# Performance work log

Hardware: AMD Instinct MI355X
Metric: run time of the kernel (lower is better)

The kernel has to match this reference:

```python
import jax, jax.numpy as jnp
import numpy as np

B, T, C = 256, 256, 147
BPM, H_DIM, NH = 32, 64, 4
HD = H_DIM // NH


def setup_inputs() -> dict:
    key = jax.random.key(0)
    ks = jax.random.split(key, 12)
    def lin(k, fan_in, fan_out):
        bound = 1.0 / np.sqrt(fan_in)
        kw, kb = jax.random.split(k)
        W = jax.random.uniform(kw, (fan_in, fan_out), jnp.float32, -bound, bound)
        b = jax.random.uniform(kb, (fan_out,), jnp.float32, -bound, bound)
        return W, b
    Wq, bq = lin(ks[0], C, H_DIM)
    Wk, bk = lin(ks[1], C, H_DIM)
    Wv, bv = lin(ks[2], C, H_DIM)
    Wb, bb = lin(ks[3], BPM, H_DIM)
    Wo, bo = lin(ks[4], H_DIM, C)
    pose = jax.random.normal(ks[5], (B, T, C), jnp.float32)
    bpm_emb = jax.random.normal(ks[6], (B, BPM), jnp.float32)
    return {"pose": pose, "bpm_emb": bpm_emb,
            "Wq": Wq, "bq": bq, "Wk": Wk, "bk": bk, "Wv": Wv, "bv": bv,
            "Wb": Wb, "bb": bb, "Wo": Wo, "bo": bo}


def reference(pose, bpm_emb, Wq, bq, Wk, bk, Wv, bv, Wb, bb, Wo, bo):
    Bb, Tt, Cc = pose.shape
    scale = HD ** -0.5
    # projections -> [B, H, T, hd]
    def split_heads(x):
        return x.reshape(Bb, Tt, NH, HD).transpose(0, 2, 1, 3)
    q = split_heads(pose @ Wq + bq)
    k = split_heads(pose @ Wk + bk)
    v = split_heads(pose @ Wv + bv)
    # bpm-conditioned key bias: [B, H, 1, hd]
    bpm_feat = (bpm_emb @ Wb + bb).reshape(Bb, 1, NH, HD).transpose(0, 2, 1, 3)
    k = k + bpm_feat
    # attention
    scores = jnp.einsum('bhqd,bhkd->bhqk', q, k) * scale
    attn = jax.nn.softmax(scores, axis=-1)
    out = jnp.einsum('bhqk,bhkd->bhqd', attn, v)
    out = out.transpose(0, 2, 1, 3).reshape(Bb, Tt, NH * HD)
    return out @ Wo + bo
```

## Files before the change

### kernel.cpp

```cpp
#include <hip/hip_runtime.h>

constexpr int kC = 147, kH = 64, kHD = 16, kBPM = 32;

typedef __attribute__((ext_vector_type(8)))  short bf16x8;
typedef __attribute__((ext_vector_type(4)))  float f32x4;
typedef __attribute__((ext_vector_type(16))) float f32x16;
typedef __attribute__((ext_vector_type(4)))  short s16x4;

__device__ __forceinline__ short f2bf(float f) {
    unsigned u = __builtin_bit_cast(unsigned, f);
    u += 0x7fffu + ((u >> 16) & 1u);
    return (short)(u >> 16);
}
#define MFMA16(a,b,c) __builtin_amdgcn_mfma_f32_16x16x32_bf16((a),(b),(c),0,0,0)
#define MFMA32(a,b,c) __builtin_amdgcn_mfma_f32_32x32x16_bf16((a),(b),(c),0,0,0)

#if __has_builtin(__builtin_amdgcn_exp2f)
  #define EXP2(x) __builtin_amdgcn_exp2f(x)
#else
  #define EXP2(x) __expf((x) * 0.6931471805599453f)
#endif
constexpr float kQScale = 0.25f * 1.4426950408889634f;

constexpr int QS  = 72;
constexpr int VS  = 264;
constexpr int PS  = 40;
constexpr int WSS = 168;
constexpr int WOS = 72;

__device__ __forceinline__ void stage_w_qkv(const float* __restrict__ W,
                                            float scale, short* Ws, int tid) {
    #pragma unroll
    for (int it = 0; it < 5; ++it) {
        const int i = it * 1024 + tid;
        const int c = i & 63, k = (i >> 6) * 2;
        const float v0 = (k     < kC) ? W[k * kH + c] * scale : 0.f;
        const float v1 = (k + 1 < kC) ? W[(k + 1) * kH + c] * scale : 0.f;
        const unsigned pack = (unsigned)(unsigned short)f2bf(v0)
                            | ((unsigned)(unsigned short)f2bf(v1) << 16);
        *(unsigned*)&Ws[c * WSS + (k ^ (((c >> 3) & 3) << 3))] = pack;
    }
}

__global__ __launch_bounds__(1024, 4) void fused_kernel(
    const float* __restrict__ pose, const float* __restrict__ bpm_emb,
    const float* __restrict__ Wq, const float* __restrict__ bq,
    const float* __restrict__ Wk, const float* __restrict__ bk,
    const float* __restrict__ Wv, const float* __restrict__ bv,
    const float* __restrict__ Wb, const float* __restrict__ bb,
    const float* __restrict__ Wo, const float* __restrict__ bo,
    float* __restrict__ out)
{
    __shared__ __align__(16) short qs[256 * QS];
    __shared__ __align__(16) short ks_[256 * QS];
    __shared__ __align__(16) short vt[kH * VS];
    __shared__ __align__(16) short WsPt[20480];
    __shared__ float l_s[16 * 64];
    __shared__ float bias_s[192];
    short* const Ws = WsPt;
    short* const Pt = WsPt;

    const int tid = threadIdx.x;
    const int w = tid >> 6, lane = tid & 63;
    const int ll = lane & 15, lq = lane >> 4;
    const int lm = lane & 31, lh = lane >> 5;
    const int b = blockIdx.x;
    const size_t pbase = (size_t)b * 256 * kC;

    bf16x8 pf[5];
    {
        const int row = w * 16 + ll;
        const float* prow = pose + pbase + (size_t)row * kC;
        #pragma unroll
        for (int ksp = 0; ksp < 5; ++ksp) {
            const int c0 = ksp * 32 + lq * 8;
            float v[8];
            if (c0 + 8 <= kC) {
                const float4 f0 = *(const float4*)(prow + c0);
                const float4 f1 = *(const float4*)(prow + c0 + 4);
                v[0]=f0.x; v[1]=f0.y; v[2]=f0.z; v[3]=f0.w;
                v[4]=f1.x; v[5]=f1.y; v[6]=f1.z; v[7]=f1.w;
            } else {
                #pragma unroll
                for (int e = 0; e < 8; ++e) v[e] = (c0 + e < kC) ? prow[c0 + e] : 0.f;
            }
            bf16x8 t;
            #pragma unroll
            for (int e = 0; e < 8; ++e) t[e] = f2bf(v[e]);
            pf[ksp] = t;
        }
    }
    if (tid < 192) {
        const int m = tid >> 6, c = tid & 63;
        float a = ((m == 0) ? bq : (m == 1) ? bk : bv)[c];
        if (m == 1) {
            a += bb[c];
            #pragma unroll
            for (int k2 = 0; k2 < kBPM; ++k2)
                a = fmaf(bpm_emb[b * kBPM + k2], Wb[k2 * kH + c], a);
        }
        if (m == 0) a *= kQScale;
        bias_s[tid] = a;
    }
    stage_w_qkv(Wq, kQScale, Ws, tid);
    __syncthreads();

    for (int m = 0; m < 3; ++m) {
        f32x4 acc[4];
        #pragma unroll
        for (int mt = 0; mt < 4; ++mt) acc[mt] = (f32x4){0.f,0.f,0.f,0.f};
        #pragma unroll
        for (int ksp = 0; ksp < 5; ++ksp)
            #pragma unroll
            for (int mt = 0; mt < 4; ++mt) {
                const int c = mt * 16 + ll;
                const int key = ((c >> 3) & 3) << 3;
                const bf16x8 wf = *(const bf16x8*)(Ws + c * WSS + ((ksp*32 + lq*8) ^ key));
                acc[mt] = MFMA16(wf, pf[ksp], acc[mt]);
            }
        __syncthreads();
        if (m == 0)      stage_w_qkv(Wk, 1.0f, Ws, tid);
        else if (m == 1) stage_w_qkv(Wv, 1.0f, Ws, tid);
        const int row = w * 16 + ll;
        #pragma unroll
        for (int mt = 0; mt < 4; ++mt) {
            const int c0 = mt * 16 + 4 * lq;
            const float4 bv4 = *(const float4*)&bias_s[m * kH + c0];
            if (m < 2) {
                s16x4 pk;
                pk[0] = f2bf(acc[mt][0] + bv4.x);
                pk[1] = f2bf(acc[mt][1] + bv4.y);
                pk[2] = f2bf(acc[mt][2] + bv4.z);
                pk[3] = f2bf(acc[mt][3] + bv4.w);
                *(s16x4*)((m == 0 ? qs : ks_) + row * QS + c0) = pk;
            } else {
                vt[(c0 + 0) * VS + row] = f2bf(acc[mt][0] + bv4.x);
                vt[(c0 + 1) * VS + row] = f2bf(acc[mt][1] + bv4.y);
                vt[(c0 + 2) * VS + row] = f2bf(acc[mt][2] + bv4.z);
                vt[(c0 + 3) * VS + row] = f2bf(acc[mt][3] + bv4.w);
            }
        }
        __syncthreads();
    }

    const int h = w & 3;
    const int q0 = (w >> 2) * 64;
    bf16x8 qf[2];
    #pragma unroll
    for (int s32 = 0; s32 < 2; ++s32)
        qf[s32] = *(const bf16x8*)(qs + (q0 + s32*32 + lm) * QS + h*16 + lh*8);

    f32x4 oacc[2][2];
    #pragma unroll
    for (int s32 = 0; s32 < 2; ++s32) {
        oacc[s32][0] = (f32x4){0.f,0.f,0.f,0.f};
        oacc[s32][1] = (f32x4){0.f,0.f,0.f,0.f};
    }
    float lp[2] = {0.f, 0.f};
    short* Pw = Pt + w * 32 * PS;
    const int wkey = ((lm >> 3) & 3) << 3;

    for (int jb = 0; jb < 8; ++jb) {
        const int j0 = jb * 32;
        const bf16x8 kf = *(const bf16x8*)(ks_ + (j0 + lm) * QS + h*16 + lh*8);
        const bf16x8 vf = *(const bf16x8*)(vt + (h*16 + ll) * VS + j0 + lq*8);
        #pragma unroll
        for (int s32 = 0; s32 < 2; ++s32) {
            const f32x16 z16 = {0.f,0.f,0.f,0.f,0.f,0.f,0.f,0.f,
                                0.f,0.f,0.f,0.f,0.f,0.f,0.f,0.f};
            const f32x16 s = MFMA32(kf, qf[s32], z16);
            float sum = 0.f;
            #pragma unroll
            for (int g = 0; g < 4; ++g) {
                const float p0 = EXP2(s[4*g + 0]);
                const float p1 = EXP2(s[4*g + 1]);
                const float p2 = EXP2(s[4*g + 2]);
                const float p3 = EXP2(s[4*g + 3]);
                sum += (p0 + p1) + (p2 + p3);
                s16x4 pk; pk[0] = f2bf(p0); pk[1] = f2bf(p1);
                pk[2] = f2bf(p2); pk[3] = f2bf(p3);
                *(s16x4*)(Pw + lm * PS + ((8*g + 4*lh) ^ wkey)) = pk;
            }
            lp[s32] += sum;
            #pragma unroll
            for (int half = 0; half < 2; ++half) {
                const int qp = half * 16 + ll;
                const int rkey = ((qp >> 3) & 3) << 3;
                const bf16x8 pfr = *(const bf16x8*)(Pw + qp * PS + ((lq*8) ^ rkey));
                oacc[s32][half] = MFMA16(vf, pfr, oacc[s32][half]);
            }
        }
    }
    #pragma unroll
    for (int s32 = 0; s32 < 2; ++s32) {
        const float l2 = lp[s32] + __shfl_xor(lp[s32], 32);
        if (lane < 32) l_s[w * 64 + s32 * 32 + lm] = l2;
    }
    #pragma unroll
    for (int s32 = 0; s32 < 2; ++s32)
        #pragma unroll
        for (int half = 0; half < 2; ++half) {
            const int qi = s32 * 32 + half * 16 + ll;
            const float inv = 1.f / l_s[w * 64 + qi];
            s16x4 pk;
            #pragma unroll
            for (int r = 0; r < 4; ++r) pk[r] = f2bf(oacc[s32][half][r] * inv);
            *(s16x4*)(qs + (q0 + qi) * QS + h*16 + 4*lq) = pk;
        }
    __syncthreads();

    #pragma unroll
    for (int it = 0; it < 5; ++it) {
        const int i = it * 1024 + tid;
        const int n = i % 160, k = (i / 160) * 2;
        const float v0 = (n < kC) ? Wo[k * kC + n] : 0.f;
        const float v1 = (n < kC) ? Wo[(k + 1) * kC + n] : 0.f;
        const unsigned pack = (unsigned)(unsigned short)f2bf(v0)
                            | ((unsigned)(unsigned short)f2bf(v1) << 16);
        *(unsigned*)&Ws[n * WOS + (k ^ (((n >> 3) & 3) << 3))] = pack;
    }
    __syncthreads();

    bf16x8 xf[2];
    #pragma unroll
    for (int k2 = 0; k2 < 2; ++k2)
        xf[k2] = *(const bf16x8*)(qs + (w*16 + ll) * QS + k2*32 + lq*8);

    f32x4 po[10];
    #pragma unroll
    for (int mt = 0; mt < 10; ++mt) po[mt] = (f32x4){0.f,0.f,0.f,0.f};
    #pragma unroll
    for (int k2 = 0; k2 < 2; ++k2)
        #pragma unroll
        for (int mt = 0; mt < 10; ++mt) {
            const int n = mt * 16 + ll;
            const int key = ((n >> 3) & 3) << 3;
            const bf16x8 wf = *(const bf16x8*)(Ws + n * WOS + ((k2*32 + lq*8) ^ key));
            po[mt] = MFMA16(wf, xf[k2], po[mt]);
        }
    {
        const int row = w * 16 + ll;
        float* orow = out + ((size_t)b * 256 + row) * kC;
        #pragma unroll
        for (int mt = 0; mt < 10; ++mt) {
            const int c0 = mt * 16 + 4 * lq;
            if (mt < 9) {
                const float4 bv4 = *(const float4*)(bo + c0);
                float4 o;
                o.x = po[mt][0] + bv4.x; o.y = po[mt][1] + bv4.y;
                o.z = po[mt][2] + bv4.z; o.w = po[mt][3] + bv4.w;
                *(float4*)(orow + c0) = o;
            } else {
                #pragma unroll
                for (int r = 0; r < 4; ++r) {
                    const int c = c0 + r;
                    if (c < kC) orow[c] = po[mt][r] + bo[c];
                }
            }
        }
    }
}

extern "C" void kernel_launch(void* const* d_in, const int* in_sizes, int n_in,
                              void* d_out, int out_size, void* d_ws, size_t ws_size,
                              hipStream_t stream) {
    const float* pose    = (const float*)d_in[0];
    const float* bpm_emb = (const float*)d_in[1];
    const float* Wq = (const float*)d_in[2];  const float* bq = (const float*)d_in[3];
    const float* Wk = (const float*)d_in[4];  const float* bk = (const float*)d_in[5];
    const float* Wv = (const float*)d_in[6];  const float* bv = (const float*)d_in[7];
    const float* Wb = (const float*)d_in[8];  const float* bb = (const float*)d_in[9];
    const float* Wo = (const float*)d_in[10]; const float* bo = (const float*)d_in[11];
    float* out = (float*)d_out;

    fused_kernel<<<256, 1024, 0, stream>>>(
        pose, bpm_emb, Wq, bq, Wk, bk, Wv, bv, Wb, bb, Wo, bo, out);
}
```

Baseline: 134.7 us.

## Split fused attention kernel into QKV projection and attention kernels via workspace

Splits the single fused per-batch kernel (256 blocks of 1024 threads) into two kernels, each with 512 blocks of 512 threads. The first computes Q, K and transposed V for half a sequence per block and writes them as bf16 to global workspace. The second computes attention plus the output projection for half the queries, reading K and V directly from global memory. This is meant to double the block count for better CU fill and cut per-block LDS use, at the cost of a global round trip for Q/K/V, a second launch, and Wo being staged twice per batch.

```diff
diff --git a/kernel.cpp b/kernel.cpp
--- a/kernel.cpp
+++ b/kernel.cpp
@@ -1,6 +1,6 @@
 #include <hip/hip_runtime.h>
 
-constexpr int kC = 147, kH = 64, kHD = 16, kBPM = 32;
+constexpr int kC = 147, kH = 64, kBPM = 32;
 
 typedef __attribute__((ext_vector_type(8)))  short bf16x8;
 typedef __attribute__((ext_vector_type(4)))  float f32x4;
@@ -23,7 +23,7 @@
 constexpr float kQScale = 0.25f * 1.4426950408889634f;
 
 constexpr int QS  = 72;
-constexpr int VS  = 264;
+constexpr int VSA = 136;
 constexpr int PS  = 40;
 constexpr int WSS = 168;
 constexpr int WOS = 72;
@@ -31,8 +31,8 @@
 __device__ __forceinline__ void stage_w_qkv(const float* __restrict__ W,
                                             float scale, short* Ws, int tid) {
     #pragma unroll
-    for (int it = 0; it < 5; ++it) {
-        const int i = it * 1024 + tid;
+    for (int it = 0; it < 10; ++it) {
+        const int i = it * 512 + tid;
         const int c = i & 63, k = (i >> 6) * 2;
         const float v0 = (k     < kC) ? W[k * kH + c] * scale : 0.f;
         const float v1 = (k + 1 < kC) ? W[(k + 1) * kH + c] * scale : 0.f;
@@ -42,34 +42,27 @@
     }
 }
 
-__global__ __launch_bounds__(1024, 4) void fused_kernel(
+__global__ __launch_bounds__(512, 4) void qkv_kernel(
     const float* __restrict__ pose, const float* __restrict__ bpm_emb,
     const float* __restrict__ Wq, const float* __restrict__ bq,
     const float* __restrict__ Wk, const float* __restrict__ bk,
     const float* __restrict__ Wv, const float* __restrict__ bv,
     const float* __restrict__ Wb, const float* __restrict__ bb,
-    const float* __restrict__ Wo, const float* __restrict__ bo,
-    float* __restrict__ out)
+    short* __restrict__ q_g, short* __restrict__ k_g, short* __restrict__ vT_g)
 {
-    __shared__ __align__(16) short qs[256 * QS];
-    __shared__ __align__(16) short ks_[256 * QS];
-    __shared__ __align__(16) short vt[kH * VS];
-    __shared__ __align__(16) short WsPt[20480];
-    __shared__ float l_s[16 * 64];
+    __shared__ __align__(16) short Ws[64 * WSS];
+    __shared__ __align__(16) short vt[64 * VSA];
     __shared__ float bias_s[192];
-    short* const Ws = WsPt;
-    short* const Pt = WsPt;
 
     const int tid = threadIdx.x;
     const int w = tid >> 6, lane = tid & 63;
     const int ll = lane & 15, lq = lane >> 4;
-    const int lm = lane & 31, lh = lane >> 5;
-    const int b = blockIdx.x;
+    const int b = blockIdx.x >> 1, half = blockIdx.x & 1;
     const size_t pbase = (size_t)b * 256 * kC;
+    const int row = half * 128 + w * 16 + ll;
 
     bf16x8 pf[5];
     {
-        const int row = w * 16 + ll;
         const float* prow = pose + pbase + (size_t)row * kC;
         #pragma unroll
         for (int ksp = 0; ksp < 5; ++ksp) {
@@ -121,7 +114,6 @@
         __syncthreads();
         if (m == 0)      stage_w_qkv(Wk, 1.0f, Ws, tid);
         else if (m == 1) stage_w_qkv(Wv, 1.0f, Ws, tid);
-        const int row = w * 16 + ll;
         #pragma unroll
         for (int mt = 0; mt < 4; ++mt) {
             const int c0 = mt * 16 + 4 * lq;
@@ -132,23 +124,54 @@
                 pk[1] = f2bf(acc[mt][1] + bv4.y);
                 pk[2] = f2bf(acc[mt][2] + bv4.z);
                 pk[3] = f2bf(acc[mt][3] + bv4.w);
-                *(s16x4*)((m == 0 ? qs : ks_) + row * QS + c0) = pk;
+                short* dst = (m == 0) ? q_g : k_g;
+                *(s16x4*)(dst + ((size_t)b * 256 + row) * kH + c0) = pk;
             } else {
-                vt[(c0 + 0) * VS + row] = f2bf(acc[mt][0] + bv4.x);
-                vt[(c0 + 1) * VS + row] = f2bf(acc[mt][1] + bv4.y);
-                vt[(c0 + 2) * VS + row] = f2bf(acc[mt][2] + bv4.z);
-                vt[(c0 + 3) * VS + row] = f2bf(acc[mt][3] + bv4.w);
+                const int jloc = w * 16 + ll;
+                vt[(c0 + 0) * VSA + jloc] = f2bf(acc[mt][0] + bv4.x);
+                vt[(c0 + 1) * VSA + jloc] = f2bf(acc[mt][1] + bv4.y);
+                vt[(c0 + 2) * VSA + jloc] = f2bf(acc[mt][2] + bv4.z);
+                vt[(c0 + 3) * VSA + jloc] = f2bf(acc[mt][3] + bv4.w);
             }
         }
         __syncthreads();
     }
 
-    const int h = w & 3;
-    const int q0 = (w >> 2) * 64;
+    {
+        const int d = tid >> 3, j16 = (tid & 7) * 16;
+        const short* src = vt + d * VSA + j16;
+        short* dst = vT_g + ((size_t)b * kH + d) * 256 + half * 128 + j16;
+        *(int4*)(dst)     = *(const int4*)(src);
+        *(int4*)(dst + 8) = *(const int4*)(src + 8);
+    }
+}
+
+__global__ __launch_bounds__(512, 4) void attn_kernel(
+    const short* __restrict__ q_g, const short* __restrict__ k_g,
+    const short* __restrict__ vT_g,
+    const float* __restrict__ Wo, const float* __restrict__ bo,
+    float* __restrict__ out)
+{
+    __shared__ __align__(16) short X[128 * QS];
+    __shared__ __align__(16) short WsPt[160 * WOS];
+    __shared__ float l_s[8 * 64];
+    short* const Ws = WsPt;
+    short* const Pt = WsPt;
+
+    const int tid = threadIdx.x;
+    const int w = tid >> 6, lane = tid & 63;
+    const int ll = lane & 15, lq = lane >> 4;
+    const int lm = lane & 31, lh = lane >> 5;
+    const int b = blockIdx.x >> 1, qh = blockIdx.x & 1;
+    const int h = w & 3, qsel = w >> 2;
+    const int qrow0 = qh * 128 + qsel * 64;
+    const size_t kvbase = (size_t)b * 256 * kH;
+
     bf16x8 qf[2];
     #pragma unroll
     for (int s32 = 0; s32 < 2; ++s32)
-        qf[s32] = *(const bf16x8*)(qs + (q0 + s32*32 + lm) * QS + h*16 + lh*8);
+        qf[s32] = *(const bf16x8*)(q_g + kvbase
+                    + (size_t)(qrow0 + s32*32 + lm) * kH + h*16 + lh*8);
 
     f32x4 oacc[2][2];
     #pragma unroll
@@ -160,10 +183,13 @@
     short* Pw = Pt + w * 32 * PS;
     const int wkey = ((lm >> 3) & 3) << 3;
 
+    #pragma unroll 2
     for (int jb = 0; jb < 8; ++jb) {
         const int j0 = jb * 32;
-        const bf16x8 kf = *(const bf16x8*)(ks_ + (j0 + lm) * QS + h*16 + lh*8);
-        const bf16x8 vf = *(const bf16x8*)(vt + (h*16 + ll) * VS + j0 + lq*8);
+        const bf16x8 kf = *(const bf16x8*)(k_g + kvbase
+                            + (size_t)(j0 + lm) * kH + h*16 + lh*8);
+        const bf16x8 vf = *(const bf16x8*)(vT_g
+                            + ((size_t)b * kH + h*16 + ll) * 256 + j0 + lq*8);
         #pragma unroll
         for (int s32 = 0; s32 < 2; ++s32) {
             const f32x16 z16 = {0.f,0.f,0.f,0.f,0.f,0.f,0.f,0.f,
@@ -183,11 +209,11 @@
             }
             lp[s32] += sum;
             #pragma unroll
-            for (int half = 0; half < 2; ++half) {
-                const int qp = half * 16 + ll;
+            for (int hf = 0; hf < 2; ++hf) {
+                const int qp = hf * 16 + ll;
                 const int rkey = ((qp >> 3) & 3) << 3;
                 const bf16x8 pfr = *(const bf16x8*)(Pw + qp * PS + ((lq*8) ^ rkey));
-                oacc[s32][half] = MFMA16(vf, pfr, oacc[s32][half]);
+                oacc[s32][hf] = MFMA16(vf, pfr, oacc[s32][hf]);
             }
         }
     }
@@ -199,19 +225,19 @@
     #pragma unroll
     for (int s32 = 0; s32 < 2; ++s32)
         #pragma unroll
-        for (int half = 0; half < 2; ++half) {
-            const int qi = s32 * 32 + half * 16 + ll;
+        for (int hf = 0; hf < 2; ++hf) {
+            const int qi = s32 * 32 + hf * 16 + ll;
             const float inv = 1.f / l_s[w * 64 + qi];
             s16x4 pk;
             #pragma unroll
-            for (int r = 0; r < 4; ++r) pk[r] = f2bf(oacc[s32][half][r] * inv);
-            *(s16x4*)(qs + (q0 + qi) * QS + h*16 + 4*lq) = pk;
+            for (int r = 0; r < 4; ++r) pk[r] = f2bf(oacc[s32][hf][r] * inv);
+            *(s16x4*)(X + (qsel * 64 + qi) * QS + h*16 + 4*lq) = pk;
         }
     __syncthreads();
 
     #pragma unroll
-    for (int it = 0; it < 5; ++it) {
-        const int i = it * 1024 + tid;
+    for (int it = 0; it < 10; ++it) {
+        const int i = it * 512 + tid;
         const int n = i % 160, k = (i / 160) * 2;
         const float v0 = (n < kC) ? Wo[k * kC + n] : 0.f;
         const float v1 = (n < kC) ? Wo[(k + 1) * kC + n] : 0.f;
@@ -224,7 +250,7 @@
     bf16x8 xf[2];
     #pragma unroll
     for (int k2 = 0; k2 < 2; ++k2)
-        xf[k2] = *(const bf16x8*)(qs + (w*16 + ll) * QS + k2*32 + lq*8);
+        xf[k2] = *(const bf16x8*)(X + (w*16 + ll) * QS + k2*32 + lq*8);
 
     f32x4 po[10];
     #pragma unroll
@@ -239,8 +265,8 @@
             po[mt] = MFMA16(wf, xf[k2], po[mt]);
         }
     {
-        const int row = w * 16 + ll;
-        float* orow = out + ((size_t)b * 256 + row) * kC;
+        const int orow_i = qh * 128 + w * 16 + ll;
+        float* orow = out + ((size_t)b * 256 + orow_i) * kC;
         #pragma unroll
         for (int mt = 0; mt < 10; ++mt) {
             const int c0 = mt * 16 + 4 * lq;
@@ -273,6 +299,11 @@
     const float* Wo = (const float*)d_in[10]; const float* bo = (const float*)d_in[11];
     float* out = (float*)d_out;
 
-    fused_kernel<<<256, 1024, 0, stream>>>(
-        pose, bpm_emb, Wq, bq, Wk, bk, Wv, bv, Wb, bb, Wo, bo, out);
-}
+    short* q_g  = (short*)d_ws;
+    short* k_g  = q_g + (size_t)256 * 256 * kH;
+    short* vT_g = k_g + (size_t)256 * 256 * kH;
+
+    qkv_kernel<<<512, 512, 0, stream>>>(
+        pose, bpm_emb, Wq, bq, Wk, bk, Wv, bv, Wb, bb, q_g, k_g, vT_g);
+    attn_kernel<<<512, 512, 0, stream>>>(q_g, k_g, vT_g, Wo, bo, out);
+}
```

New measurement: 147.4 us. 9.4% more time.

## Prefetch weights into registers early and use hardware packed bf16 conversion

Applied to the files above, without the earlier changes.

Issues the global loads for Wq/Wk/Wv at kernel start and for Wo before the attention loop, holding them in registers so later LDS staging only converts and stores. This hides global-memory latency that previously stalled between phases. It also swaps the software round-to-nearest f2bf for the v_cvt_pk_bf16_f32 instruction in most places and unrolls the QKV and attention loops. The cost is about 40 extra live VGPRs per thread, which risks spilling under launch_bounds(1024,4).

```diff
diff --git a/kernel.cpp b/kernel.cpp
--- a/kernel.cpp
+++ b/kernel.cpp
@@ -1,16 +1,22 @@
 #include <hip/hip_runtime.h>
 
-constexpr int kC = 147, kH = 64, kHD = 16, kBPM = 32;
+constexpr int kC = 147, kH = 64, kBPM = 32;
 
 typedef __attribute__((ext_vector_type(8)))  short bf16x8;
 typedef __attribute__((ext_vector_type(4)))  float f32x4;
 typedef __attribute__((ext_vector_type(16))) float f32x16;
-typedef __attribute__((ext_vector_type(4)))  short s16x4;
+typedef __attribute__((ext_vector_type(2)))  unsigned u32x2;
+typedef __attribute__((ext_vector_type(4)))  unsigned u32x4;
 
 __device__ __forceinline__ short f2bf(float f) {
     unsigned u = __builtin_bit_cast(unsigned, f);
     u += 0x7fffu + ((u >> 16) & 1u);
     return (short)(u >> 16);
+}
+__device__ __forceinline__ unsigned cvt_pk(float lo, float hi) {
+    unsigned r;
+    asm("v_cvt_pk_bf16_f32 %0, %1, %2" : "=v"(r) : "v"(lo), "v"(hi));
+    return r;
 }
 #define MFMA16(a,b,c) __builtin_amdgcn_mfma_f32_16x16x32_bf16((a),(b),(c),0,0,0)
 #define MFMA32(a,b,c) __builtin_amdgcn_mfma_f32_32x32x16_bf16((a),(b),(c),0,0,0)
@@ -28,17 +34,14 @@
 constexpr int WSS = 168;
 constexpr int WOS = 72;
 
-__device__ __forceinline__ void stage_w_qkv(const float* __restrict__ W,
-                                            float scale, short* Ws, int tid) {
+__device__ __forceinline__ void stage_w_regs(const float* wr ,
+                                             short* Ws, int tid) {
     #pragma unroll
     for (int it = 0; it < 5; ++it) {
         const int i = it * 1024 + tid;
         const int c = i & 63, k = (i >> 6) * 2;
-        const float v0 = (k     < kC) ? W[k * kH + c] * scale : 0.f;
-        const float v1 = (k + 1 < kC) ? W[(k + 1) * kH + c] * scale : 0.f;
-        const unsigned pack = (unsigned)(unsigned short)f2bf(v0)
-                            | ((unsigned)(unsigned short)f2bf(v1) << 16);
-        *(unsigned*)&Ws[c * WSS + (k ^ (((c >> 3) & 3) << 3))] = pack;
+        *(unsigned*)&Ws[c * WSS + (k ^ (((c >> 3) & 3) << 3))]
+            = cvt_pk(wr[2*it], wr[2*it + 1]);
     }
 }
 
@@ -67,6 +70,20 @@
     const int b = blockIdx.x;
     const size_t pbase = (size_t)b * 256 * kC;
 
+    float wq_r[10], wk_r[10], wv_r[10];
+    #pragma unroll
+    for (int it = 0; it < 5; ++it) {
+        const int i = it * 1024 + tid;
+        const int c = i & 63, k = (i >> 6) * 2;
+        const bool b0 = k < kC, b1 = k + 1 < kC;
+        wq_r[2*it]   = b0 ? Wq[k * kH + c] * kQScale : 0.f;
+        wq_r[2*it+1] = b1 ? Wq[(k + 1) * kH + c] * kQScale : 0.f;
+        wk_r[2*it]   = b0 ? Wk[k * kH + c] : 0.f;
+        wk_r[2*it+1] = b1 ? Wk[(k + 1) * kH + c] : 0.f;
+        wv_r[2*it]   = b0 ? Wv[k * kH + c] : 0.f;
+        wv_r[2*it+1] = b1 ? Wv[(k + 1) * kH + c] : 0.f;
+    }
+
     bf16x8 pf[5];
     {
         const int row = w * 16 + ll;
@@ -84,10 +101,9 @@
                 #pragma unroll
                 for (int e = 0; e < 8; ++e) v[e] = (c0 + e < kC) ? prow[c0 + e] : 0.f;
             }
-            bf16x8 t;
-            #pragma unroll
-            for (int e = 0; e < 8; ++e) t[e] = f2bf(v[e]);
-            pf[ksp] = t;
+            const u32x4 t = { cvt_pk(v[0], v[1]), cvt_pk(v[2], v[3]),
+                              cvt_pk(v[4], v[5]), cvt_pk(v[6], v[7]) };
+            pf[ksp] = __builtin_bit_cast(bf16x8, t);
         }
     }
     if (tid < 192) {
@@ -102,9 +118,10 @@
         if (m == 0) a *= kQScale;
         bias_s[tid] = a;
     }
-    stage_w_qkv(Wq, kQScale, Ws, tid);
+    stage_w_regs(wq_r, Ws, tid);
     __syncthreads();
 
+    #pragma unroll
     for (int m = 0; m < 3; ++m) {
         f32x4 acc[4];
         #pragma unroll
@@ -119,20 +136,17 @@
                 acc[mt] = MFMA16(wf, pf[ksp], acc[mt]);
             }
         __syncthreads();
-        if (m == 0)      stage_w_qkv(Wk, 1.0f, Ws, tid);
-        else if (m == 1) stage_w_qkv(Wv, 1.0f, Ws, tid);
+        if (m == 0)      stage_w_regs(wk_r, Ws, tid);
+        else if (m == 1) stage_w_regs(wv_r, Ws, tid);
         const int row = w * 16 + ll;
         #pragma unroll
         for (int mt = 0; mt < 4; ++mt) {
             const int c0 = mt * 16 + 4 * lq;
             const float4 bv4 = *(const float4*)&bias_s[m * kH + c0];
             if (m < 2) {
-                s16x4 pk;
-                pk[0] = f2bf(acc[mt][0] + bv4.x);
-                pk[1] = f2bf(acc[mt][1] + bv4.y);
-                pk[2] = f2bf(acc[mt][2] + bv4.z);
-                pk[3] = f2bf(acc[mt][3] + bv4.w);
-                *(s16x4*)((m == 0 ? qs : ks_) + row * QS + c0) = pk;
+                const u32x2 pk = { cvt_pk(acc[mt][0] + bv4.x, acc[mt][1] + bv4.y),
+                                   cvt_pk(acc[mt][2] + bv4.z, acc[mt][3] + bv4.w) };
+                *(u32x2*)((m == 0 ? qs : ks_) + row * QS + c0) = pk;
             } else {
                 vt[(c0 + 0) * VS + row] = f2bf(acc[mt][0] + bv4.x);
                 vt[(c0 + 1) * VS + row] = f2bf(acc[mt][1] + bv4.y);
@@ -150,6 +164,15 @@
     for (int s32 = 0; s32 < 2; ++s32)
         qf[s32] = *(const bf16x8*)(qs + (q0 + s32*32 + lm) * QS + h*16 + lh*8);
 
+    float wo_r[10];
+    #pragma unroll
+    for (int it = 0; it < 5; ++it) {
+        const int i = it * 1024 + tid;
+        const int n = i % 160, k = (i / 160) * 2;
+        wo_r[2*it]   = (n < kC) ? Wo[k * kC + n] : 0.f;
+        wo_r[2*it+1] = (n < kC) ? Wo[(k + 1) * kC + n] : 0.f;
+    }
+
     f32x4 oacc[2][2];
     #pragma unroll
     for (int s32 = 0; s32 < 2; ++s32) {
@@ -160,6 +183,7 @@
     short* Pw = Pt + w * 32 * PS;
     const int wkey = ((lm >> 3) & 3) << 3;
 
+    #pragma unroll 2
     for (int jb = 0; jb < 8; ++jb) {
         const int j0 = jb * 32;
         const bf16x8 kf = *(const bf16x8*)(ks_ + (j0 + lm) * QS + h*16 + lh*8);
@@ -177,9 +201,8 @@
                 const float p2 = EXP2(s[4*g + 2]);
                 const float p3 = EXP2(s[4*g + 3]);
                 sum += (p0 + p1) + (p2 + p3);
-                s16x4 pk; pk[0] = f2bf(p0); pk[1] = f2bf(p1);
-                pk[2] = f2bf(p2); pk[3] = f2bf(p3);
-                *(s16x4*)(Pw + lm * PS + ((8*g + 4*lh) ^ wkey)) = pk;
+                const u32x2 pk = { cvt_pk(p0, p1), cvt_pk(p2, p3) };
+                *(u32x2*)(Pw + lm * PS + ((8*g + 4*lh) ^ wkey)) = pk;
             }
             lp[s32] += sum;
             #pragma unroll
@@ -202,10 +225,9 @@
         for (int half = 0; half < 2; ++half) {
             const int qi = s32 * 32 + half * 16 + ll;
             const float inv = 1.f / l_s[w * 64 + qi];
-            s16x4 pk;
-            #pragma unroll
-            for (int r = 0; r < 4; ++r) pk[r] = f2bf(oacc[s32][half][r] * inv);
-            *(s16x4*)(qs + (q0 + qi) * QS + h*16 + 4*lq) = pk;
+            const u32x2 pk = { cvt_pk(oacc[s32][half][0] * inv, oacc[s32][half][1] * inv),
+                               cvt_pk(oacc[s32][half][2] * inv, oacc[s32][half][3] * inv) };
+            *(u32x2*)(qs + (q0 + qi) * QS + h*16 + 4*lq) = pk;
         }
     __syncthreads();
 
@@ -213,11 +235,8 @@
     for (int it = 0; it < 5; ++it) {
         const int i = it * 1024 + tid;
         const int n = i % 160, k = (i / 160) * 2;
-        const float v0 = (n < kC) ? Wo[k * kC + n] : 0.f;
-        const float v1 = (n < kC) ? Wo[(k + 1) * kC + n] : 0.f;
-        const unsigned pack = (unsigned)(unsigned short)f2bf(v0)
-                            | ((unsigned)(unsigned short)f2bf(v1) << 16);
-        *(unsigned*)&Ws[n * WOS + (k ^ (((n >> 3) & 3) << 3))] = pack;
+        *(unsigned*)&Ws[n * WOS + (k ^ (((n >> 3) & 3) << 3))]
+            = cvt_pk(wo_r[2*it], wo_r[2*it + 1]);
     }
     __syncthreads();
 
```

After: 129.1 us. 4.2% less time.
